# Kernel optimization log

Hardware: AMD Instinct MI355X
Metric: run time of the kernel (lower is better)

## Reference

```python
import jax, jax.numpy as jnp
import numpy as np

B, S, D, H = 2, 2048, 512, 8
HD = D // H
EPS = 1e-5


def _ln(x, g, b):
    mu = jnp.mean(x, axis=-1, keepdims=True)
    var = jnp.mean((x - mu) ** 2, axis=-1, keepdims=True)
    return (x - mu) * jax.lax.rsqrt(var + EPS) * g + b


def setup_inputs() -> dict:
    key = jax.random.key(0)
    ks = jax.random.split(key, 16)
    x = jax.random.normal(ks[0], (B, S, D), dtype=jnp.float32)
    adj = jax.random.randint(ks[1], (B, S, S), 0, 2, dtype=jnp.int32)
    adj = adj.at[:, jnp.arange(S), jnp.arange(S)].set(1)  # self-loops, avoid all-masked rows
    edge_attr = jax.random.normal(ks[2], (B, S, S), dtype=jnp.float32)
    sc = 1.0 / np.sqrt(D)
    p = lambda k, shp: jax.random.normal(k, shp, dtype=jnp.float32) * sc
    return {
        "x": x, "adj_matrix": adj, "edge_attr_matrix": edge_attr,
        "ln1_g": jnp.ones((D,)), "ln1_b": jnp.zeros((D,)),
        "ln2_g": jnp.ones((D,)), "ln2_b": jnp.zeros((D,)),
        "wq": p(ks[3], (D, D)), "bq": jnp.zeros((D,)),
        "wk": p(ks[4], (D, D)), "bk": jnp.zeros((D,)),
        "wv": p(ks[5], (D, D)), "bv": jnp.zeros((D,)),
        "wo": p(ks[6], (D, D)), "bo": jnp.zeros((D,)),
        "w1": p(ks[7], (D, 4 * D)), "b1": jnp.zeros((4 * D,)),
        "w2": p(ks[8], (4 * D, D)), "b2": jnp.zeros((D,)),
    }


def reference(x, adj_matrix, edge_attr_matrix, ln1_g, ln1_b, ln2_g, ln2_b,
              wq, bq, wk, bk, wv, bv, wo, bo, w1, b1, w2, b2):
    b, s, d = x.shape
    residual = x
    nx = _ln(x, ln1_g, ln1_b)
    q = (nx @ wq + bq).reshape(b, s, H, HD).transpose(0, 2, 1, 3)  # [B,H,S,HD]
    k = (nx @ wk + bk).reshape(b, s, H, HD).transpose(0, 2, 1, 3)
    v = (nx @ wv + bv).reshape(b, s, H, HD).transpose(0, 2, 1, 3)
    adjf = adj_matrix.astype(jnp.float32)
    # bias: -inf where no edge, else 0.1*edge_attr*adj (faithful to score_mod)
    bias = jnp.where(adj_matrix > 0, 0.1 * edge_attr_matrix * adjf, -jnp.inf)[:, None]  # [B,1,S,S]
    scores = jnp.einsum('bhqd,bhkd->bhqk', q, k) / np.sqrt(HD) + bias
    attn = jax.nn.softmax(scores, axis=-1)
    out = jnp.einsum('bhqk,bhkd->bhqd', attn, v)
    out = out.transpose(0, 2, 1, 3).reshape(b, s, d)
    x1 = residual + (out @ wo + bo)
    n2 = _ln(x1, ln2_g, ln2_b)
    mlp = jax.nn.gelu(n2 @ w1 + b1, approximate=False) @ w2 + b2
    return x1 + mlp
```

## Files before the change

kernel.cpp:

```cpp
#include <hip/hip_runtime.h>
#include <cstdint>
#include <cstddef>

typedef __bf16 bf16x8 __attribute__((ext_vector_type(8)));
typedef float f32x4 __attribute__((ext_vector_type(4)));
typedef const __attribute__((address_space(1))) void* gas_t;
typedef __attribute__((address_space(3))) void* las_t;

#define QSCALE 0.18033688011112042f
#define BSCALE 0.14426950408889634f

__device__ __forceinline__ unsigned short f2bf(float f) {
  union { float f; unsigned u; } v; v.f = f;
  unsigned r = v.u + 0x7FFFu + ((v.u >> 16) & 1u);
  return (unsigned short)(r >> 16);
}
__device__ __forceinline__ unsigned short f2bf_fast(float f) {
  union { float f; unsigned u; } v; v.f = f;
  return (unsigned short)((v.u + 0x8000u) >> 16);
}
__device__ __forceinline__ float bf2f(unsigned short h) {
  union { unsigned u; float f; } v; v.u = ((unsigned)h) << 16;
  return v.f;
}
__device__ __forceinline__ void gll16(const void* g, void* l) {
  __builtin_amdgcn_global_load_lds((gas_t)g, (las_t)l, 16, 0, 0);
}

__global__ __launch_bounds__(256) void transpose_cast(const float* __restrict__ in,
                                                      unsigned short* __restrict__ out,
                                                      int R, int C) {
  __shared__ float tile[32][33];
  int bx = blockIdx.x * 32, by = blockIdx.y * 32;
  int tx = threadIdx.x & 31, tg = threadIdx.x >> 5;
  #pragma unroll
  for (int i = 0; i < 4; i++) {
    int r = tg * 4 + i;
    tile[r][tx] = in[(size_t)(by + r) * C + bx + tx];
  }
  __syncthreads();
  #pragma unroll
  for (int i = 0; i < 4; i++) {
    int r = tg * 4 + i;
    out[(size_t)(bx + r) * R + by + tx] = f2bf(tile[tx][r]);
  }
}

struct TP4 { const float* in[4]; unsigned short* out[4]; };
__global__ __launch_bounds__(256) void transpose_cast4(TP4 p) {
  __shared__ float tile[32][33];
  const float* in = p.in[blockIdx.z];
  unsigned short* out = p.out[blockIdx.z];
  int bx = blockIdx.x * 32, by = blockIdx.y * 32;
  int tx = threadIdx.x & 31, tg = threadIdx.x >> 5;
  #pragma unroll
  for (int i = 0; i < 4; i++) {
    int r = tg * 4 + i;
    tile[r][tx] = in[(size_t)(by + r) * 512 + bx + tx];
  }
  __syncthreads();
  #pragma unroll
  for (int i = 0; i < 4; i++) {
    int r = tg * 4 + i;
    out[(size_t)(bx + r) * 512 + by + tx] = f2bf(tile[tx][r]);
  }
}

__global__ __launch_bounds__(256) void bias_pack(const int* __restrict__ adj,
                                                 const float* __restrict__ edge,
                                                 unsigned short* __restrict__ bp) {
  size_t i = ((size_t)blockIdx.x * 256 + threadIdx.x) * 4;
  int4 a = *(const int4*)(adj + i);
  float4 e = *(const float4*)(edge + i);
  ushort4 r;
  r.x = a.x > 0 ? f2bf(BSCALE * e.x * (float)a.x - 20.0f) : f2bf(-30000.0f);
  r.y = a.y > 0 ? f2bf(BSCALE * e.y * (float)a.y - 20.0f) : f2bf(-30000.0f);
  r.z = a.z > 0 ? f2bf(BSCALE * e.z * (float)a.z - 20.0f) : f2bf(-30000.0f);
  r.w = a.w > 0 ? f2bf(BSCALE * e.w * (float)a.w - 20.0f) : f2bf(-30000.0f);
  *(ushort4*)(bp + i) = r;
}

__global__ __launch_bounds__(256) void ln_kernel(const float* __restrict__ x,
                                                 const float* __restrict__ g,
                                                 const float* __restrict__ bt,
                                                 unsigned short* __restrict__ out) {
  int row = blockIdx.x, tid = threadIdx.x;
  float2 v = *(const float2*)(x + (size_t)row * 512 + tid * 2);
  float s = v.x + v.y, s2 = v.x * v.x + v.y * v.y;
  #pragma unroll
  for (int m = 1; m < 64; m <<= 1) { s += __shfl_xor(s, m, 64); s2 += __shfl_xor(s2, m, 64); }
  __shared__ float red[8];
  int w = tid >> 6;
  if ((tid & 63) == 0) { red[w * 2] = s; red[w * 2 + 1] = s2; }
  __syncthreads();
  float ts = red[0] + red[2] + red[4] + red[6];
  float ts2 = red[1] + red[3] + red[5] + red[7];
  float mu = ts * (1.0f / 512.0f);
  float rs = rsqrtf(ts2 * (1.0f / 512.0f) - mu * mu + 1e-5f);
  int c = tid * 2;
  ushort2 o;
  o.x = f2bf((v.x - mu) * rs * g[c] + bt[c]);
  o.y = f2bf((v.y - mu) * rs * g[c + 1] + bt[c + 1]);
  *(ushort2*)(out + (size_t)row * 512 + c) = o;
}

__global__ __launch_bounds__(256) void ln_fuse2(const float* __restrict__ x,
                                                const unsigned short* __restrict__ opp,
                                                const float* __restrict__ bo,
                                                const float* __restrict__ g,
                                                const float* __restrict__ bt,
                                                float* __restrict__ x1,
                                                unsigned short* __restrict__ n2) {
  const size_t MN = (size_t)4096 * 512;
  int row = blockIdx.x, tid = threadIdx.x;
  int c = tid * 2;
  size_t idx = (size_t)row * 512 + c;
  float2 xv = *(const float2*)(x + idx);
  ushort2 p0 = *(const ushort2*)(opp + idx);
  ushort2 p1 = *(const ushort2*)(opp + MN + idx);
  float2 v;
  v.x = xv.x + bo[c]     + bf2f(p0.x) + bf2f(p1.x);
  v.y = xv.y + bo[c + 1] + bf2f(p0.y) + bf2f(p1.y);
  float s = v.x + v.y, s2 = v.x * v.x + v.y * v.y;
  #pragma unroll
  for (int m = 1; m < 64; m <<= 1) { s += __shfl_xor(s, m, 64); s2 += __shfl_xor(s2, m, 64); }
  __shared__ float red[8];
  int w = tid >> 6;
  if ((tid & 63) == 0) { red[w * 2] = s; red[w * 2 + 1] = s2; }
  __syncthreads();
  float ts = red[0] + red[2] + red[4] + red[6];
  float ts2 = red[1] + red[3] + red[5] + red[7];
  float mu = ts * (1.0f / 512.0f);
  float rs = rsqrtf(ts2 * (1.0f / 512.0f) - mu * mu + 1e-5f);
  *(float2*)(x1 + idx) = v;
  ushort2 o;
  o.x = f2bf((v.x - mu) * rs * g[c] + bt[c]);
  o.y = f2bf((v.y - mu) * rs * g[c + 1] + bt[c + 1]);
  *(ushort2*)(n2 + idx) = o;
}

__global__ __launch_bounds__(256) void final_combine(const float* __restrict__ x1,
                                                     const float* __restrict__ b2,
                                                     const unsigned short* __restrict__ mp,
                                                     float* __restrict__ out) {
  const size_t MN = (size_t)4096 * 512;
  size_t i = ((size_t)blockIdx.x * 256 + threadIdx.x) * 4;
  float4 xv = *(const float4*)(x1 + i);
  float4 bv = *(const float4*)(b2 + (i & 511));
  float4 a;
  a.x = xv.x + bv.x; a.y = xv.y + bv.y; a.z = xv.z + bv.z; a.w = xv.w + bv.w;
  #pragma unroll
  for (int sp = 0; sp < 4; sp++) {
    ushort4 p = *(const ushort4*)(mp + sp * MN + i);
    a.x += bf2f(p.x); a.y += bf2f(p.y); a.z += bf2f(p.z); a.w += bf2f(p.w);
  }
  *(float4*)(out + i) = a;
}

struct EpiQKV {
  unsigned short *q, *k, *v;
  const float *bq, *bk, *bv;
  __device__ void operator()(int m, int n, float val) const {
    int b = m >> 11, s = m & 2047;
    int which = n >> 9, col = n & 511;
    int h = col >> 6, d = col & 63;
    int bh = b * 8 + h;
    if (which == 0)      q[((size_t)bh * 2048 + s) * 64 + d] = f2bf((val + bq[col]) * QSCALE);
    else if (which == 1) k[((size_t)bh * 2048 + s) * 64 + d] = f2bf(val + bk[col]);
    else                 v[((size_t)bh * 2048 + s) * 64 + d] = f2bf(val + bv[col]);
  }
};
struct EpiPart {
  unsigned short* dst; int ldn;
  __device__ void operator()(int m, int n, float val) const {
    dst[(size_t)blockIdx.z * 4096 * 512 + (size_t)m * ldn + n] = f2bf(val);
  }
};
struct EpiGelu {
  const float* b1; unsigned short* h;
  __device__ void operator()(int m, int n, float val) const {
    float t = val + b1[n];
    float gl = 0.5f * t * (1.0f + erff(t * 0.70710678118654752f));
    h[(size_t)m * 2048 + n] = f2bf(gl);
  }
};

template <typename Epi>
__global__ __launch_bounds__(256) void gemm_bt(const unsigned short* __restrict__ A,
                                               const unsigned short* __restrict__ Bt,
                                               int lda, int ldb, int kchunk, Epi epi) {
  __shared__ unsigned short a_lds[128 * 64];
  __shared__ unsigned short b_lds[128 * 64];
  const int tid = threadIdx.x;
  const int lane = tid & 63;
  const int w = tid >> 6;
  const int l15 = lane & 15, quad = lane >> 4;
  const int wm = w >> 1, wn = w & 1;
  const int m0 = blockIdx.y * 128, n0 = blockIdx.x * 128;
  const int K0 = blockIdx.z * kchunk, K1 = K0 + kchunk;

  f32x4 acc[4][4] = {};

  for (int k0 = K0; k0 < K1; k0 += 64) {
    __syncthreads();
    #pragma unroll
    for (int i = 0; i < 4; i++) {
      int c = tid + i * 256;
      int g = c >> 6;
      int row = (g >> 1) * 16 + l15;
      int col = (g & 1) * 32 + quad * 8;
      gll16(A + (size_t)(m0 + row) * lda + k0 + col, a_lds + (size_t)(c & ~63) * 8);
      gll16(Bt + (size_t)(n0 + row) * ldb + k0 + col, b_lds + (size_t)(c & ~63) * 8);
    }
    __syncthreads();
    bf16x8 af[4][2], bfr[4][2];
    #pragma unroll
    for (int t = 0; t < 4; t++)
      #pragma unroll
      for (int ks = 0; ks < 2; ks++) {
        af[t][ks]  = *(const bf16x8*)(a_lds + (((size_t)(wm * 4 + t) * 2 + ks) * 64 + lane) * 8);
        bfr[t][ks] = *(const bf16x8*)(b_lds + (((size_t)(wn * 4 + t) * 2 + ks) * 64 + lane) * 8);
      }
    #pragma unroll
    for (int mt = 0; mt < 4; mt++)
      #pragma unroll
      for (int nt = 0; nt < 4; nt++) {
        acc[mt][nt] = __builtin_amdgcn_mfma_f32_16x16x32_bf16(af[mt][0], bfr[nt][0], acc[mt][nt], 0, 0, 0);
        acc[mt][nt] = __builtin_amdgcn_mfma_f32_16x16x32_bf16(af[mt][1], bfr[nt][1], acc[mt][nt], 0, 0, 0);
      }
  }
  #pragma unroll
  for (int mt = 0; mt < 4; mt++)
    #pragma unroll
    for (int nt = 0; nt < 4; nt++)
      #pragma unroll
      for (int r = 0; r < 4; r++)
        epi(m0 + wm * 64 + mt * 16 + quad * 4 + r, n0 + wn * 64 + nt * 16 + l15, acc[mt][nt][r]);
}

__global__ __launch_bounds__(256) void vt_kernel(const unsigned short* __restrict__ vb,
                                                 unsigned short* __restrict__ vbT) {
  __shared__ unsigned short tile[64][72];
  const int bh = blockIdx.y, s0 = blockIdx.x * 64;
  const int tid = threadIdx.x;
  const unsigned short* src = vb + ((size_t)bh * 2048 + s0) * 64;
  #pragma unroll
  for (int i = 0; i < 2; i++) {
    int r = (tid >> 3) + i * 32;
    int c8 = (tid & 7) * 8;
    *(uint4*)(&tile[r][c8]) = *(const uint4*)(src + (size_t)r * 64 + c8);
  }
  __syncthreads();
  unsigned short* dst = vbT + (size_t)bh * 64 * 2048 + s0;
  #pragma unroll
  for (int i = 0; i < 2; i++) {
    int d = (tid >> 3) + i * 32;
    int s8 = (tid & 7) * 8;
    ushort4 o0, o1;
    o0.x = tile[s8 + 0][d]; o0.y = tile[s8 + 1][d]; o0.z = tile[s8 + 2][d]; o0.w = tile[s8 + 3][d];
    o1.x = tile[s8 + 4][d]; o1.y = tile[s8 + 5][d]; o1.z = tile[s8 + 6][d]; o1.w = tile[s8 + 7][d];
    *(ushort4*)(dst + (size_t)d * 2048 + s8) = o0;
    *(ushort4*)(dst + (size_t)d * 2048 + s8 + 4) = o1;
  }
}

__global__ __launch_bounds__(256, 4) void attn_kernel(const unsigned short* __restrict__ Q,
                                                      const unsigned short* __restrict__ Kb,
                                                      const unsigned short* __restrict__ VT,
                                                      const unsigned short* __restrict__ biasp,
                                                      unsigned short* __restrict__ o_part,
                                                      float* __restrict__ l_part) {
  __shared__ unsigned short k_lds[64 * 64];
  __shared__ unsigned short v_lds[64 * 64];
  __shared__ unsigned short p_lds[4][2][16 * 72];

  const int tid = threadIdx.x;
  const int lane = tid & 63, w = tid >> 6;
  const int l15 = lane & 15, quad = lane >> 4;
  const int bh = blockIdx.x, b = bh >> 3;
  const int q0 = blockIdx.y * 128;
  const int split = blockIdx.z;

  bf16x8 qf[2][2];
  const unsigned short* brow[2];
  #pragma unroll
  for (int g = 0; g < 2; g++) {
    const unsigned short* qrow = Q + ((size_t)bh * 2048 + q0 + w * 32 + g * 16 + l15) * 64;
    qf[g][0] = *(const bf16x8*)(qrow + quad * 8);
    qf[g][1] = *(const bf16x8*)(qrow + 32 + quad * 8);
    brow[g] = biasp + ((size_t)b * 2048 + q0 + w * 32 + g * 16 + l15) * 2048;
  }

  f32x4 o_acc[2][4] = {};
  float l_acc[2] = {0.0f, 0.0f};

  const unsigned short* kbase = Kb + (size_t)bh * 2048 * 64;
  const unsigned short* vbase = VT + (size_t)bh * 64 * 2048;

  const int kt0 = split * 8, kt1 = kt0 + 8;
  for (int kt = kt0; kt < kt1; kt++) {
    const int kcol0 = kt * 64;
    __syncthreads();
    #pragma unroll
    for (int i = 0; i < 2; i++) {
      int c = tid + i * 256;
      int g = c >> 6;
      int mt = g >> 1, kk = g & 1;
      int rr = mt * 16 + l15;
      int cc = kk * 32 + quad * 8;
      gll16(kbase + (size_t)(kcol0 + rr) * 64 + cc, k_lds + (size_t)(c & ~63) * 8);
      gll16(vbase + (size_t)rr * 2048 + kcol0 + cc, v_lds + (size_t)(c & ~63) * 8);
    }
    ushort4 bl[2][4];
    #pragma unroll
    for (int g = 0; g < 2; g++)
      #pragma unroll
      for (int mt = 0; mt < 4; mt++)
        bl[g][mt] = *(const ushort4*)(brow[g] + kcol0 + mt * 16 + quad * 4);
    __syncthreads();

    #pragma unroll
    for (int mt = 0; mt < 4; mt++) {
      bf16x8 a0 = *(const bf16x8*)(k_lds + ((size_t)(mt * 2 + 0) * 64 + lane) * 8);
      bf16x8 a1 = *(const bf16x8*)(k_lds + ((size_t)(mt * 2 + 1) * 64 + lane) * 8);
      #pragma unroll
      for (int g = 0; g < 2; g++) {
        f32x4 cb;
        cb[0] = bf2f(bl[g][mt].x); cb[1] = bf2f(bl[g][mt].y);
        cb[2] = bf2f(bl[g][mt].z); cb[3] = bf2f(bl[g][mt].w);
        f32x4 accv = __builtin_amdgcn_mfma_f32_16x16x32_bf16(a0, qf[g][0], cb, 0, 0, 0);
        accv = __builtin_amdgcn_mfma_f32_16x16x32_bf16(a1, qf[g][1], accv, 0, 0, 0);
        float p0 = exp2f(accv[0]), p1 = exp2f(accv[1]);
        float p2 = exp2f(accv[2]), p3 = exp2f(accv[3]);
        l_acc[g] += (p0 + p1) + (p2 + p3);
        ushort4 pv;
        pv.x = f2bf_fast(p0); pv.y = f2bf_fast(p1); pv.z = f2bf_fast(p2); pv.w = f2bf_fast(p3);
        *(ushort4*)(p_lds[w][g] + l15 * 72 + mt * 16 + quad * 4) = pv;
      }
    }

    bf16x8 pf[2][2];
    #pragma unroll
    for (int g = 0; g < 2; g++) {
      pf[g][0] = *(const bf16x8*)(p_lds[w][g] + l15 * 72 + quad * 8);
      pf[g][1] = *(const bf16x8*)(p_lds[w][g] + l15 * 72 + 32 + quad * 8);
    }
    #pragma unroll
    for (int dt = 0; dt < 4; dt++) {
      bf16x8 v0 = *(const bf16x8*)(v_lds + ((size_t)(dt * 2 + 0) * 64 + lane) * 8);
      bf16x8 v1 = *(const bf16x8*)(v_lds + ((size_t)(dt * 2 + 1) * 64 + lane) * 8);
      #pragma unroll
      for (int g = 0; g < 2; g++) {
        o_acc[g][dt] = __builtin_amdgcn_mfma_f32_16x16x32_bf16(pf[g][0], v0, o_acc[g][dt], 0, 0, 0);
        o_acc[g][dt] = __builtin_amdgcn_mfma_f32_16x16x32_bf16(pf[g][1], v1, o_acc[g][dt], 0, 0, 0);
      }
    }
  }

  const size_t obase = ((size_t)split * 16 + bh) * 2048;
  #pragma unroll
  for (int g = 0; g < 2; g++) {
    float l = l_acc[g];
    l += __shfl_xor(l, 16, 64);
    l += __shfl_xor(l, 32, 64);
    if (quad == 0) l_part[obase + q0 + w * 32 + g * 16 + l15] = l;
    #pragma unroll
    for (int dt = 0; dt < 4; dt++)
      #pragma unroll
      for (int r = 0; r < 4; r++)
        o_part[(obase + q0 + w * 32 + g * 16 + quad * 4 + r) * 64 + dt * 16 + l15] =
            f2bf(o_acc[g][dt][r]);
  }
}

__global__ __launch_bounds__(256) void combine_kernel(const unsigned short* __restrict__ o_part,
                                                      const float* __restrict__ l_part,
                                                      unsigned short* __restrict__ ao) {
  const int row = blockIdx.x;
  const int b = row >> 11, s = row & 2047;
  const int col = threadIdx.x * 2;
  const int h = col >> 6, d = col & 63;
  const int bh = b * 8 + h;
  float ox = 0.0f, oy = 0.0f, l = 0.0f;
  #pragma unroll
  for (int sp = 0; sp < 4; sp++) {
    size_t base = (size_t)(sp * 16 + bh) * 2048 + s;
    ushort2 o = *(const ushort2*)(o_part + base * 64 + d);
    ox += bf2f(o.x); oy += bf2f(o.y);
    l += l_part[base];
  }
  float inv = 1.0f / l;
  ushort2 o;
  o.x = f2bf(ox * inv);
  o.y = f2bf(oy * inv);
  *(ushort2*)(ao + (size_t)row * 512 + col) = o;
}

extern "C" void kernel_launch(void* const* d_in, const int* in_sizes, int n_in,
                              void* d_out, int out_size, void* d_ws, size_t ws_size,
                              hipStream_t stream) {
  (void)in_sizes; (void)n_in; (void)out_size; (void)ws_size;
  const float* x    = (const float*)d_in[0];
  const int*   adj  = (const int*)d_in[1];
  const float* edge = (const float*)d_in[2];
  const float* ln1g = (const float*)d_in[3];
  const float* ln1b = (const float*)d_in[4];
  const float* ln2g = (const float*)d_in[5];
  const float* ln2b = (const float*)d_in[6];
  const float* wq = (const float*)d_in[7];  const float* bq = (const float*)d_in[8];
  const float* wk = (const float*)d_in[9];  const float* bk = (const float*)d_in[10];
  const float* wv = (const float*)d_in[11]; const float* bv = (const float*)d_in[12];
  const float* wo = (const float*)d_in[13]; const float* bo = (const float*)d_in[14];
  const float* w1 = (const float*)d_in[15]; const float* b1 = (const float*)d_in[16];
  const float* w2 = (const float*)d_in[17]; const float* b2 = (const float*)d_in[18];
  float* out = (float*)d_out;

  char* ws = (char*)d_ws;
  unsigned short* qkvT = (unsigned short*)ws; ws += (size_t)1536 * 512 * 2;
  unsigned short* woT  = (unsigned short*)ws; ws += (size_t)512 * 512 * 2;
  unsigned short* w1T  = (unsigned short*)ws; ws += (size_t)2048 * 512 * 2;
  unsigned short* w2T  = (unsigned short*)ws; ws += (size_t)512 * 2048 * 2;
  unsigned short* bp   = (unsigned short*)ws;
  unsigned short* opp  = (unsigned short*)ws; ws += (size_t)2 * 2048 * 2048 * 2;
  unsigned short* nx   = (unsigned short*)ws;
  unsigned short* n2   = (unsigned short*)ws; ws += (size_t)4096 * 512 * 2;
  unsigned short* qb   = (unsigned short*)ws;
  unsigned short* ao   = (unsigned short*)ws; ws += (size_t)4096 * 512 * 2;
  unsigned short* kb   = (unsigned short*)ws; ws += (size_t)4096 * 512 * 2;
  unsigned short* vb   = (unsigned short*)ws;
  float*          x1   = (float*)ws;          ws += (size_t)4096 * 512 * 2;
  unsigned short* vbT  = (unsigned short*)ws; ws += (size_t)4096 * 512 * 2;
  char* region1 = ws;
  unsigned short* opt  = (unsigned short*)region1;
  unsigned short* hb   = (unsigned short*)region1;
  float*          lpt  = (float*)(region1 + (size_t)4 * 16 * 2048 * 64 * 2);
  unsigned short* mp   = (unsigned short*)(region1 + (size_t)4 * 16 * 2048 * 64 * 2);

  dim3 blk(256);
  TP4 tp; tp.in[0] = wq; tp.in[1] = wk; tp.in[2] = wv; tp.in[3] = wo;
  tp.out[0] = qkvT; tp.out[1] = qkvT + (size_t)512 * 512;
  tp.out[2] = qkvT + (size_t)2 * 512 * 512; tp.out[3] = woT;
  transpose_cast4<<<dim3(16, 16, 4), blk, 0, stream>>>(tp);
  transpose_cast<<<dim3(64, 16), blk, 0, stream>>>(w1, w1T, 512, 2048);
  transpose_cast<<<dim3(16, 64), blk, 0, stream>>>(w2, w2T, 2048, 512);
  bias_pack<<<8192, blk, 0, stream>>>(adj, edge, bp);
  ln_kernel<<<4096, blk, 0, stream>>>(x, ln1g, ln1b, nx);
  gemm_bt<<<dim3(12, 32, 1), blk, 0, stream>>>(nx, qkvT, 512, 512, 512,
                                               EpiQKV{qb, kb, vb, bq, bk, bv});
  vt_kernel<<<dim3(32, 16), blk, 0, stream>>>(vb, vbT);
  attn_kernel<<<dim3(16, 16, 4), blk, 0, stream>>>(qb, kb, vbT, bp, opt, lpt);
  combine_kernel<<<4096, blk, 0, stream>>>(opt, lpt, ao);
  gemm_bt<<<dim3(4, 32, 2), blk, 0, stream>>>(ao, woT, 512, 512, 256,
                                              EpiPart{opp, 512});
  ln_fuse2<<<4096, blk, 0, stream>>>(x, opp, bo, ln2g, ln2b, x1, n2);
  gemm_bt<<<dim3(16, 32, 1), blk, 0, stream>>>(n2, w1T, 512, 512, 512,
                                               EpiGelu{b1, hb});
  gemm_bt<<<dim3(4, 32, 4), blk, 0, stream>>>(hb, w2T, 2048, 2048, 512,
                                              EpiPart{mp, 512});
  final_combine<<<2048, blk, 0, stream>>>(x1, b2, mp, out);
}
```

Before: 321.7 us.

## Double-buffer LDS in GEMM and attention, cut attention key splits to three

```diff
diff --git a/kernel.cpp b/kernel.cpp
--- a/kernel.cpp
+++ b/kernel.cpp
@@ -186,40 +186,54 @@
 };
 
 template <typename Epi>
-__global__ __launch_bounds__(256) void gemm_bt(const unsigned short* __restrict__ A,
-                                               const unsigned short* __restrict__ Bt,
-                                               int lda, int ldb, int kchunk, Epi epi) {
-  __shared__ unsigned short a_lds[128 * 64];
-  __shared__ unsigned short b_lds[128 * 64];
+__global__ __launch_bounds__(256, 2) void gemm_bt(const unsigned short* __restrict__ A,
+                                                  const unsigned short* __restrict__ Bt,
+                                                  int lda, int ldb, int kchunk, Epi epi) {
+  __shared__ unsigned short a_lds[2][128 * 64];
+  __shared__ unsigned short b_lds[2][128 * 64];
   const int tid = threadIdx.x;
   const int lane = tid & 63;
   const int w = tid >> 6;
   const int l15 = lane & 15, quad = lane >> 4;
   const int wm = w >> 1, wn = w & 1;
   const int m0 = blockIdx.y * 128, n0 = blockIdx.x * 128;
-  const int K0 = blockIdx.z * kchunk, K1 = K0 + kchunk;
+  const int K0 = blockIdx.z * kchunk;
+  const int nIter = kchunk >> 6;
 
   f32x4 acc[4][4] = {};
 
-  for (int k0 = K0; k0 < K1; k0 += 64) {
+  #pragma unroll
+  for (int i = 0; i < 4; i++) {
+    int c = tid + i * 256;
+    int g = c >> 6;
+    int row = (g >> 1) * 16 + l15;
+    int col = (g & 1) * 32 + quad * 8;
+    gll16(A + (size_t)(m0 + row) * lda + K0 + col, a_lds[0] + (size_t)(c & ~63) * 8);
+    gll16(Bt + (size_t)(n0 + row) * ldb + K0 + col, b_lds[0] + (size_t)(c & ~63) * 8);
+  }
+
+  for (int it = 0; it < nIter; it++) {
+    const int cur = it & 1;
     __syncthreads();
-    #pragma unroll
-    for (int i = 0; i < 4; i++) {
-      int c = tid + i * 256;
-      int g = c >> 6;
-      int row = (g >> 1) * 16 + l15;
-      int col = (g & 1) * 32 + quad * 8;
-      gll16(A + (size_t)(m0 + row) * lda + k0 + col, a_lds + (size_t)(c & ~63) * 8);
-      gll16(Bt + (size_t)(n0 + row) * ldb + k0 + col, b_lds + (size_t)(c & ~63) * 8);
+    if (it + 1 < nIter) {
+      const int kn = K0 + (it + 1) * 64;
+      #pragma unroll
+      for (int i = 0; i < 4; i++) {
+        int c = tid + i * 256;
+        int g = c >> 6;
+        int row = (g >> 1) * 16 + l15;
+        int col = (g & 1) * 32 + quad * 8;
+        gll16(A + (size_t)(m0 + row) * lda + kn + col, a_lds[1 - cur] + (size_t)(c & ~63) * 8);
+        gll16(Bt + (size_t)(n0 + row) * ldb + kn + col, b_lds[1 - cur] + (size_t)(c & ~63) * 8);
+      }
     }
-    __syncthreads();
     bf16x8 af[4][2], bfr[4][2];
     #pragma unroll
     for (int t = 0; t < 4; t++)
       #pragma unroll
       for (int ks = 0; ks < 2; ks++) {
-        af[t][ks]  = *(const bf16x8*)(a_lds + (((size_t)(wm * 4 + t) * 2 + ks) * 64 + lane) * 8);
-        bfr[t][ks] = *(const bf16x8*)(b_lds + (((size_t)(wn * 4 + t) * 2 + ks) * 64 + lane) * 8);
+        af[t][ks]  = *(const bf16x8*)(a_lds[cur] + (((size_t)(wm * 4 + t) * 2 + ks) * 64 + lane) * 8);
+        bfr[t][ks] = *(const bf16x8*)(b_lds[cur] + (((size_t)(wn * 4 + t) * 2 + ks) * 64 + lane) * 8);
       }
     #pragma unroll
     for (int mt = 0; mt < 4; mt++)
@@ -264,15 +278,15 @@
   }
 }
 
-__global__ __launch_bounds__(256, 4) void attn_kernel(const unsigned short* __restrict__ Q,
+__global__ __launch_bounds__(256, 3) void attn_kernel(const unsigned short* __restrict__ Q,
                                                       const unsigned short* __restrict__ Kb,
                                                       const unsigned short* __restrict__ VT,
                                                       const unsigned short* __restrict__ biasp,
                                                       unsigned short* __restrict__ o_part,
                                                       float* __restrict__ l_part) {
-  __shared__ unsigned short k_lds[64 * 64];
-  __shared__ unsigned short v_lds[64 * 64];
-  __shared__ unsigned short p_lds[4][2][16 * 72];
+  __shared__ unsigned short k_lds[2][64 * 64];
+  __shared__ unsigned short v_lds[2][64 * 64];
+  __shared__ unsigned short p_lds[4][2][16 * 68];
 
   const int tid = threadIdx.x;
   const int lane = tid & 63, w = tid >> 6;
@@ -297,37 +311,55 @@
   const unsigned short* kbase = Kb + (size_t)bh * 2048 * 64;
   const unsigned short* vbase = VT + (size_t)bh * 64 * 2048;
 
-  const int kt0 = split * 8, kt1 = kt0 + 8;
+  const int kt0 = split * 11;
+  const int kt1 = (kt0 + 11 < 32) ? kt0 + 11 : 32;
+
+  #pragma unroll
+  for (int i = 0; i < 2; i++) {
+    int c = tid + i * 256;
+    int g = c >> 6;
+    int rr = (g >> 1) * 16 + l15;
+    int cc = (g & 1) * 32 + quad * 8;
+    gll16(kbase + (size_t)(kt0 * 64 + rr) * 64 + cc, k_lds[0] + (size_t)(c & ~63) * 8);
+    gll16(vbase + (size_t)rr * 2048 + kt0 * 64 + cc, v_lds[0] + (size_t)(c & ~63) * 8);
+  }
+  ushort4 blc[2][4];
+  #pragma unroll
+  for (int g = 0; g < 2; g++)
+    #pragma unroll
+    for (int mt = 0; mt < 4; mt++)
+      blc[g][mt] = *(const ushort4*)(brow[g] + kt0 * 64 + mt * 16 + quad * 4);
+
   for (int kt = kt0; kt < kt1; kt++) {
-    const int kcol0 = kt * 64;
+    const int cur = (kt - kt0) & 1;
     __syncthreads();
+
+    const int ktn = (kt + 1 < kt1) ? kt + 1 : kt;
     #pragma unroll
     for (int i = 0; i < 2; i++) {
       int c = tid + i * 256;
       int g = c >> 6;
-      int mt = g >> 1, kk = g & 1;
-      int rr = mt * 16 + l15;
-      int cc = kk * 32 + quad * 8;
-      gll16(kbase + (size_t)(kcol0 + rr) * 64 + cc, k_lds + (size_t)(c & ~63) * 8);
-      gll16(vbase + (size_t)rr * 2048 + kcol0 + cc, v_lds + (size_t)(c & ~63) * 8);
+      int rr = (g >> 1) * 16 + l15;
+      int cc = (g & 1) * 32 + quad * 8;
+      gll16(kbase + (size_t)(ktn * 64 + rr) * 64 + cc, k_lds[1 - cur] + (size_t)(c & ~63) * 8);
+      gll16(vbase + (size_t)rr * 2048 + ktn * 64 + cc, v_lds[1 - cur] + (size_t)(c & ~63) * 8);
     }
-    ushort4 bl[2][4];
+    ushort4 bln[2][4];
     #pragma unroll
     for (int g = 0; g < 2; g++)
       #pragma unroll
       for (int mt = 0; mt < 4; mt++)
-        bl[g][mt] = *(const ushort4*)(brow[g] + kcol0 + mt * 16 + quad * 4);
-    __syncthreads();
+        bln[g][mt] = *(const ushort4*)(brow[g] + ktn * 64 + mt * 16 + quad * 4);
 
     #pragma unroll
     for (int mt = 0; mt < 4; mt++) {
-      bf16x8 a0 = *(const bf16x8*)(k_lds + ((size_t)(mt * 2 + 0) * 64 + lane) * 8);
-      bf16x8 a1 = *(const bf16x8*)(k_lds + ((size_t)(mt * 2 + 1) * 64 + lane) * 8);
+      bf16x8 a0 = *(const bf16x8*)(k_lds[cur] + ((size_t)(mt * 2 + 0) * 64 + lane) * 8);
+      bf16x8 a1 = *(const bf16x8*)(k_lds[cur] + ((size_t)(mt * 2 + 1) * 64 + lane) * 8);
       #pragma unroll
       for (int g = 0; g < 2; g++) {
         f32x4 cb;
-        cb[0] = bf2f(bl[g][mt].x); cb[1] = bf2f(bl[g][mt].y);
-        cb[2] = bf2f(bl[g][mt].z); cb[3] = bf2f(bl[g][mt].w);
+        cb[0] = bf2f(blc[g][mt].x); cb[1] = bf2f(blc[g][mt].y);
+        cb[2] = bf2f(blc[g][mt].z); cb[3] = bf2f(blc[g][mt].w);
         f32x4 accv = __builtin_amdgcn_mfma_f32_16x16x32_bf16(a0, qf[g][0], cb, 0, 0, 0);
         accv = __builtin_amdgcn_mfma_f32_16x16x32_bf16(a1, qf[g][1], accv, 0, 0, 0);
         float p0 = exp2f(accv[0]), p1 = exp2f(accv[1]);
@@ -335,26 +367,32 @@
         l_acc[g] += (p0 + p1) + (p2 + p3);
         ushort4 pv;
         pv.x = f2bf_fast(p0); pv.y = f2bf_fast(p1); pv.z = f2bf_fast(p2); pv.w = f2bf_fast(p3);
-        *(ushort4*)(p_lds[w][g] + l15 * 72 + mt * 16 + quad * 4) = pv;
+        *(ushort4*)(p_lds[w][g] + l15 * 68 + mt * 16 + quad * 4) = pv;
       }
     }
 
     bf16x8 pf[2][2];
     #pragma unroll
     for (int g = 0; g < 2; g++) {
-      pf[g][0] = *(const bf16x8*)(p_lds[w][g] + l15 * 72 + quad * 8);
-      pf[g][1] = *(const bf16x8*)(p_lds[w][g] + l15 * 72 + 32 + quad * 8);
+      pf[g][0] = *(const bf16x8*)(p_lds[w][g] + l15 * 68 + quad * 8);
+      pf[g][1] = *(const bf16x8*)(p_lds[w][g] + l15 * 68 + 32 + quad * 8);
     }
     #pragma unroll
     for (int dt = 0; dt < 4; dt++) {
-      bf16x8 v0 = *(const bf16x8*)(v_lds + ((size_t)(dt * 2 + 0) * 64 + lane) * 8);
-      bf16x8 v1 = *(const bf16x8*)(v_lds + ((size_t)(dt * 2 + 1) * 64 + lane) * 8);
+      bf16x8 v0 = *(const bf16x8*)(v_lds[cur] + ((size_t)(dt * 2 + 0) * 64 + lane) * 8);
+      bf16x8 v1 = *(const bf16x8*)(v_lds[cur] + ((size_t)(dt * 2 + 1) * 64 + lane) * 8);
       #pragma unroll
       for (int g = 0; g < 2; g++) {
         o_acc[g][dt] = __builtin_amdgcn_mfma_f32_16x16x32_bf16(pf[g][0], v0, o_acc[g][dt], 0, 0, 0);
         o_acc[g][dt] = __builtin_amdgcn_mfma_f32_16x16x32_bf16(pf[g][1], v1, o_acc[g][dt], 0, 0, 0);
       }
     }
+
+    #pragma unroll
+    for (int g = 0; g < 2; g++)
+      #pragma unroll
+      for (int mt = 0; mt < 4; mt++)
+        blc[g][mt] = bln[g][mt];
   }
 
   const size_t obase = ((size_t)split * 16 + bh) * 2048;
@@ -383,7 +421,7 @@
   const int bh = b * 8 + h;
   float ox = 0.0f, oy = 0.0f, l = 0.0f;
   #pragma unroll
-  for (int sp = 0; sp < 4; sp++) {
+  for (int sp = 0; sp < 3; sp++) {
     size_t base = (size_t)(sp * 16 + bh) * 2048 + s;
     ushort2 o = *(const ushort2*)(o_part + base * 64 + d);
     ox += bf2f(o.x); oy += bf2f(o.y);
@@ -433,8 +471,8 @@
   char* region1 = ws;
   unsigned short* opt  = (unsigned short*)region1;
   unsigned short* hb   = (unsigned short*)region1;
-  float*          lpt  = (float*)(region1 + (size_t)4 * 16 * 2048 * 64 * 2);
-  unsigned short* mp   = (unsigned short*)(region1 + (size_t)4 * 16 * 2048 * 64 * 2);
+  float*          lpt  = (float*)(region1 + (size_t)3 * 16 * 2048 * 64 * 2);
+  unsigned short* mp   = (unsigned short*)(region1 + (size_t)16777216);
 
   dim3 blk(256);
   TP4 tp; tp.in[0] = wq; tp.in[1] = wk; tp.in[2] = wv; tp.in[3] = wo;
@@ -448,7 +486,7 @@
   gemm_bt<<<dim3(12, 32, 1), blk, 0, stream>>>(nx, qkvT, 512, 512, 512,
                                                EpiQKV{qb, kb, vb, bq, bk, bv});
   vt_kernel<<<dim3(32, 16), blk, 0, stream>>>(vb, vbT);
-  attn_kernel<<<dim3(16, 16, 4), blk, 0, stream>>>(qb, kb, vbT, bp, opt, lpt);
+  attn_kernel<<<dim3(16, 16, 3), blk, 0, stream>>>(qb, kb, vbT, bp, opt, lpt);
   combine_kernel<<<4096, blk, 0, stream>>>(opt, lpt, ao);
   gemm_bt<<<dim3(4, 32, 2), blk, 0, stream>>>(ao, woT, 512, 512, 256,
                                               EpiPart{opp, 512});
```

After: 317.6 us. About the same (-1.3%).
